# Performance work log

Hardware: AMD Instinct MI355X
Metric: run time of the kernel (lower is better)

Reference implementation:

```python
import jax, jax.numpy as jnp
import numpy as np

B = 2048        # graphs per batch
NC = 81         # cells per sudoku
IN_C, HID = 10, 128
N_ACT, N_NUM, N_TECH = 4, 9, 10


def _sudoku_edges():
    idx = np.arange(NC).reshape(9, 9)
    adj = np.zeros((NC, NC), dtype=bool)
    for i in range(9):
        for j in range(9):
            n = idx[i, j]
            adj[n, idx[i, :]] = True
            adj[n, idx[:, j]] = True
            bi, bj = 3 * (i // 3), 3 * (j // 3)
            adj[n, idx[bi:bi + 3, bj:bj + 3].reshape(-1)] = True
            adj[n, n] = False
    src, dst = np.nonzero(adj)  # 1620 directed edges
    return np.stack([src, dst]).astype(np.int32)


def setup_inputs() -> dict:
    key = jax.random.key(0)
    ks = jax.random.split(key, 12)
    N = B * NC
    base = _sudoku_edges()                          # [2, 1620]
    offs = (np.arange(B, dtype=np.int32) * NC)      # [B]
    ei = (base[:, None, :] + offs[None, :, None]).reshape(2, -1)  # [2, B*1620]
    batch = np.repeat(np.arange(B, dtype=np.int32), NC)           # [N]

    def lin(k, fan_in, fan_out):
        s = 1.0 / np.sqrt(fan_in)
        return jax.random.uniform(k, (fan_in, fan_out), jnp.float32, -s, s)

    return {
        "x": jax.random.normal(ks[0], (N, IN_C), jnp.float32),
        "edge_index": jnp.asarray(ei),
        "batch": jnp.asarray(batch),
        "W1": lin(ks[1], IN_C, HID), "b1": jnp.zeros((HID,), jnp.float32),
        "W2": lin(ks[2], HID, HID),  "b2": jnp.zeros((HID,), jnp.float32),
        "Wa": lin(ks[3], HID, N_ACT),  "ba": jnp.zeros((N_ACT,), jnp.float32),
        "Wc": lin(ks[4], HID, NC),     "bc": jnp.zeros((NC,), jnp.float32),
        "Wn": lin(ks[5], HID, N_NUM),  "bn": jnp.zeros((N_NUM,), jnp.float32),
        "Wt": lin(ks[6], HID, N_TECH), "bt": jnp.zeros((N_TECH,), jnp.float32),
    }


def _gcn_conv(x, edge_index, W, b):
    n = x.shape[0]
    loop = jnp.arange(n, dtype=edge_index.dtype)
    src = jnp.concatenate([edge_index[0], loop])
    dst = jnp.concatenate([edge_index[1], loop])
    deg = jax.ops.segment_sum(jnp.ones_like(dst, jnp.float32), dst, num_segments=n)
    dinv = jax.lax.rsqrt(deg)            # deg >= 1 due to self-loops
    norm = dinv[src] * dinv[dst]         # [E+N]
    h = x @ W                            # [N, out]
    msg = h[src] * norm[:, None]         # gather + scale
    return jax.ops.segment_sum(msg, dst, num_segments=n) + b


def reference(x, edge_index, batch, W1, b1, W2, b2, Wa, ba, Wc, bc, Wn, bn, Wt, bt):
    h = jax.nn.relu(_gcn_conv(x, edge_index, W1, b1))
    h = jax.nn.relu(_gcn_conv(h, edge_index, W2, b2))
    # global mean pool over graphs
    sums = jax.ops.segment_sum(h, batch, num_segments=B)
    cnts = jax.ops.segment_sum(jnp.ones((h.shape[0],), h.dtype), batch, num_segments=B)
    pooled = sums / jnp.maximum(cnts, 1.0)[:, None]   # [B, HID]
    return (pooled @ Wa + ba, pooled @ Wc + bc, pooled @ Wn + bn, pooled @ Wt + bt)
```

## Files before the change

kernel.cpp:

```cpp
#include <hip/hip_runtime.h>
#include <hip/hip_bf16.h>

typedef __attribute__((ext_vector_type(8))) short bf16x8;
typedef __attribute__((ext_vector_type(4))) float f32x4;

__device__ __forceinline__ unsigned short f2b(float f) {
    __hip_bfloat16 h = __float2bfloat16(f);
    return __builtin_bit_cast(unsigned short, h);
}
__device__ __forceinline__ float b2f(unsigned short u) {
    unsigned v = ((unsigned)u) << 16;
    return __builtin_bit_cast(float, v);
}
__device__ __forceinline__ float ldf(const void* p, int idx, bool f32) {
    return f32 ? ((const float*)p)[idx] : b2f(((const unsigned short*)p)[idx]);
}
__device__ __forceinline__ unsigned short ldb(const void* p, int idx, bool f32) {
    return f32 ? f2b(((const float*)p)[idx]) : ((const unsigned short*)p)[idx];
}
__device__ __forceinline__ int swz(int row, int col) {
    return row * 128 + (((col >> 3) ^ (row & 7)) << 3) + (col & 7);
}
__device__ __forceinline__ uint2 pk4(f32x4 c) {
    unsigned lo = (unsigned)f2b(c[0]) | ((unsigned)f2b(c[1]) << 16);
    unsigned hi = (unsigned)f2b(c[2]) | ((unsigned)f2b(c[3]) << 16);
    return make_uint2(lo, hi);
}
__device__ __forceinline__ bf16x8 mkB(uint2 a, uint2 b) {
    return __builtin_bit_cast(bf16x8, make_uint4(a.x, a.y, b.x, b.y));
}

__device__ __forceinline__ bool sniff_f32(const void* x) {
    const unsigned* p = (const unsigned*)x;
    int wild = 0;
#pragma unroll
    for (int i = 0; i < 16; ++i) {
        unsigned e = (p[i] >> 7) & 0xFF;
        wild += (e != 0 && (e < 0x68 || e > 0x90)) ? 1 : 0;
    }
    return wild > 8;
}

#define WS_B1F    16
#define WS_B2F    528
#define WS_BHF    1040
#define WS_W1R    1536
#define WS_W2R    9728
#define WS_SR     42496
#define WS_WH     60928

__global__ void k_repack(const void* __restrict__ x,
                         const void* __restrict__ W1, const void* __restrict__ b1,
                         const void* __restrict__ W2, const void* __restrict__ b2,
                         const void* __restrict__ Wa, const void* __restrict__ ba,
                         const void* __restrict__ Wc, const void* __restrict__ bc,
                         const void* __restrict__ Wn, const void* __restrict__ bn,
                         const void* __restrict__ Wt, const void* __restrict__ bt,
                         char* __restrict__ ws) {
    const bool f32 = sniff_f32(x);
    int idx = blockIdx.x * blockDim.x + threadIdx.x;
    if (idx < 4096) {
        int f = idx >> 5, k = idx & 31;
        unsigned short v = (k < 10) ? ldb(W1, k * 128 + f, f32) : (unsigned short)0;
        ((unsigned short*)(ws + WS_W1R))[idx] = v;
        return;
    }
    idx -= 4096;
    if (idx < 16384) {
        int f = idx >> 7, k = idx & 127;
        ((unsigned short*)(ws + WS_W2R))[idx] = ldb(W2, k * 128 + f, f32);
        return;
    }
    idx -= 16384;
    if (idx < 9216) {
        int fi = idx >> 9, rem = idx & 511;
        int lane = rem >> 3, j = rem & 7;
        int mt = fi / 3, s = fi - mt * 3;
        int node = mt * 16 + (lane & 15);
        int qa = lane >> 4;
        int cell = (2 * s + (j >> 2)) * 16 + qa * 4 + (j & 3);
        bool adj = false;
        if (node < 81 && cell < 81) {
            int ni = node / 9, nj = node % 9;
            int ci = cell / 9, cj = cell % 9;
            adj = (ni == ci) || (nj == cj) ||
                  ((ni / 3 == ci / 3) && (nj / 3 == cj / 3));
        }
        ((unsigned short*)(ws + WS_SR))[idx] = adj ? (unsigned short)0x3F80 : (unsigned short)0;
        return;
    }
    idx -= 9216;
    if (idx < 13312) {
        int i = idx / 416;
        int rem = idx - i * 416;
        int o = rem >> 2;
        int c = rem & 3;
        int f = i * 4 + c;
        const void* W; int oo, dim;
        if (o < 4)       { W = Wa; oo = o;      dim = 4;  }
        else if (o < 85) { W = Wc; oo = o - 4;  dim = 81; }
        else if (o < 94) { W = Wn; oo = o - 85; dim = 9;  }
        else             { W = Wt; oo = o - 94; dim = 10; }
        ((float*)(ws + WS_WH))[idx] = ldf(W, f * dim + oo, f32);
        return;
    }
    idx -= 13312;
    if (idx < 360) {
        float v;
        if (idx < 128)      v = ldf(b1, idx, f32);
        else if (idx < 256) v = ldf(b2, idx - 128, f32);
        else {
            int o = idx - 256;
            if (o < 4)       v = ldf(ba, o, f32);
            else if (o < 85) v = ldf(bc, o - 4, f32);
            else if (o < 94) v = ldf(bn, o - 85, f32);
            else             v = ldf(bt, o - 94, f32);
        }
        if (idx < 128)      ((float*)(ws + WS_B1F))[idx] = v;
        else if (idx < 256) ((float*)(ws + WS_B2F))[idx - 128] = v;
        else                ((float*)(ws + WS_BHF))[idx - 256] = v;
    }
}

__global__ __launch_bounds__(512, 4) void sudoku_gnn(
    const void* __restrict__ x, const char* __restrict__ ws,
    void* __restrict__ out, int nB)
{
    __shared__ __attribute__((aligned(16))) unsigned short hS[2][12288];
    __shared__ __attribute__((aligned(16))) unsigned short sS[9216];
    __shared__ float sPool[2][128];

    const bool f32 = sniff_f32(x);
    const unsigned short* w1r = (const unsigned short*)(ws + WS_W1R);
    const unsigned short* w2r = (const unsigned short*)(ws + WS_W2R);
    const float* b1f = (const float*)(ws + WS_B1F);
    const float* b2f = (const float*)(ws + WS_B2F);
    const float* bhf = (const float*)(ws + WS_BHF);
    const float* whf = (const float*)(ws + WS_WH);

    const int tid  = threadIdx.x;
    const int wave = tid >> 6;
    const int gq   = wave >> 2;
    const int lane = tid & 63;
    const int ln15 = lane & 15;
    const int q    = lane >> 4;
    const int k0   = q * 8;
    const int FB   = (wave & 3) * 32;
    const int g0   = blockIdx.x * 2;
    const bool hasB = (g0 + 1 < nB);
    const int g    = (g0 + gq < nB) ? g0 + gq : nB - 1;
    const float inv21 = 1.0f / 21.0f;
    const float inv81 = 1.0f / 81.0f;

    uint4 xr4[6]; unsigned xr1[6];
    if (!f32) {
        const char* xg = (const char*)x + (size_t)g * 1620;
#pragma unroll
        for (int mt = 0; mt < 6; ++mt) {
            int node = mt * 16 + ln15;
            uint4 r = {0, 0, 0, 0}; unsigned r1v = 0;
            if (node < 81) {
                if (q == 0)      r   = *(const uint4*)(xg + node * 20);
                else if (q == 1) r1v = *(const unsigned*)(xg + node * 20 + 16);
            }
            xr4[mt] = r; xr1[mt] = r1v;
        }
    }

    {
        const uint4* src = (const uint4*)(ws + WS_SR);
        uint4* dst = (uint4*)sS;
        for (int i = tid; i < 1152; i += 512) dst[i] = src[i];
    }

    bf16x8 w1f[2];
#pragma unroll
    for (int fmt = 0; fmt < 2; ++fmt)
        w1f[fmt] = *(const bf16x8*)&w1r[(FB + fmt * 16 + ln15) * 32 + k0];

    const f32x4 z4 = {0.f, 0.f, 0.f, 0.f};

    uint2 tpk[6][2];
#pragma unroll
    for (int mt = 0; mt < 6; ++mt) {
        bf16x8 xv = {0, 0, 0, 0, 0, 0, 0, 0};
        if (!f32) {
            if (q == 0)      xv = __builtin_bit_cast(bf16x8, xr4[mt]);
            else if (q == 1) { xv[0] = (short)(xr1[mt] & 0xFFFF); xv[1] = (short)(xr1[mt] >> 16); }
        } else {
            int node = mt * 16 + ln15;
            if (node < 81) {
                const float* xg = (const float*)x + (size_t)g * 810 + node * 10;
                if (q == 0) {
#pragma unroll
                    for (int j = 0; j < 8; ++j) xv[j] = (short)f2b(xg[j]);
                } else if (q == 1) {
                    xv[0] = (short)f2b(xg[8]);
                    xv[1] = (short)f2b(xg[9]);
                }
            }
        }
#pragma unroll
        for (int fmt = 0; fmt < 2; ++fmt)
            tpk[mt][fmt] = pk4(__builtin_amdgcn_mfma_f32_16x16x32_bf16(xv, w1f[fmt], z4, 0, 0, 0));
    }
    __syncthreads();

    f32x4 acc[6][2];

#pragma unroll
    for (int a = 0; a < 6; ++a)
#pragma unroll
        for (int c = 0; c < 2; ++c) acc[a][c] = z4;
    __builtin_amdgcn_s_setprio(1);
#pragma unroll
    for (int s = 0; s < 3; ++s) {
        bf16x8 B[2];
#pragma unroll
        for (int fmt = 0; fmt < 2; ++fmt)
            B[fmt] = mkB(tpk[2 * s][fmt], tpk[2 * s + 1][fmt]);
#pragma unroll
        for (int mt = 0; mt < 6; ++mt) {
            bf16x8 afr = *(const bf16x8*)&sS[((mt * 3 + s) * 64 + lane) * 8];
#pragma unroll
            for (int fmt = 0; fmt < 2; ++fmt)
                acc[mt][fmt] = __builtin_amdgcn_mfma_f32_16x16x32_bf16(afr, B[fmt], acc[mt][fmt], 0, 0, 0);
        }
    }
    __builtin_amdgcn_s_setprio(0);
#pragma unroll
    for (int fmt = 0; fmt < 2; ++fmt) {
        float bias = b1f[FB + fmt * 16 + ln15];
#pragma unroll
        for (int mt = 0; mt < 6; ++mt)
#pragma unroll
            for (int r = 0; r < 4; ++r) {
                int cell = mt * 16 + q * 4 + r;
                float v = fmaxf(acc[mt][fmt][r] * inv21 + bias, 0.0f);
                hS[gq][swz(cell, FB + fmt * 16 + ln15)] = f2b(v);
            }
    }
    __syncthreads();

#pragma unroll
    for (int a = 0; a < 6; ++a)
#pragma unroll
        for (int c = 0; c < 2; ++c) acc[a][c] = z4;
    __builtin_amdgcn_s_setprio(1);
#pragma unroll
    for (int kc = 0; kc < 4; ++kc) {
        bf16x8 w2f[2];
#pragma unroll
        for (int fmt = 0; fmt < 2; ++fmt)
            w2f[fmt] = *(const bf16x8*)&w2r[(FB + fmt * 16 + ln15) * 128 + kc * 32 + k0];
#pragma unroll
        for (int mt = 0; mt < 6; ++mt) {
            bf16x8 a3 = *(const bf16x8*)&hS[gq][swz(mt * 16 + ln15, kc * 32 + k0)];
#pragma unroll
            for (int fmt = 0; fmt < 2; ++fmt)
                acc[mt][fmt] = __builtin_amdgcn_mfma_f32_16x16x32_bf16(a3, w2f[fmt], acc[mt][fmt], 0, 0, 0);
        }
    }
    __builtin_amdgcn_s_setprio(0);
#pragma unroll
    for (int mt = 0; mt < 6; ++mt)
#pragma unroll
        for (int fmt = 0; fmt < 2; ++fmt)
            tpk[mt][fmt] = pk4(acc[mt][fmt]);

#pragma unroll
    for (int a = 0; a < 6; ++a)
#pragma unroll
        for (int c = 0; c < 2; ++c) acc[a][c] = z4;
    __builtin_amdgcn_s_setprio(1);
#pragma unroll
    for (int s = 0; s < 3; ++s) {
        bf16x8 B[2];
#pragma unroll
        for (int fmt = 0; fmt < 2; ++fmt)
            B[fmt] = mkB(tpk[2 * s][fmt], tpk[2 * s + 1][fmt]);
#pragma unroll
        for (int mt = 0; mt < 6; ++mt) {
            bf16x8 afr = *(const bf16x8*)&sS[((mt * 3 + s) * 64 + lane) * 8];
#pragma unroll
            for (int fmt = 0; fmt < 2; ++fmt)
                acc[mt][fmt] = __builtin_amdgcn_mfma_f32_16x16x32_bf16(afr, B[fmt], acc[mt][fmt], 0, 0, 0);
        }
    }
    __builtin_amdgcn_s_setprio(0);
#pragma unroll
    for (int fmt = 0; fmt < 2; ++fmt) {
        float bias = b2f[FB + fmt * 16 + ln15];
        float sum = 0.f;
#pragma unroll
        for (int mt = 0; mt < 6; ++mt)
#pragma unroll
            for (int r = 0; r < 4; ++r) {
                int cell = mt * 16 + q * 4 + r;
                float v = fmaxf(acc[mt][fmt][r] * inv21 + bias, 0.0f);
                sum += (cell < 81) ? v : 0.0f;
            }
        sum += __shfl_xor(sum, 16);
        sum += __shfl_xor(sum, 32);
        if (lane < 16) sPool[gq][FB + fmt * 16 + lane] = sum * inv81;
    }
    __syncthreads();

    if (tid < 416) {
        int pr = tid >> 1, hf = tid & 1;
        int gg = (pr >= 104) ? 1 : 0;
        int o  = pr - gg * 104;
        int gh = g0 + gg;
        float a = 0.0f;
        if (gg == 0 || hasB) {
            a = hf ? 0.0f : bhf[o];
            const float4* wh4 = (const float4*)whf;
            const float4* sp4 = (const float4*)sPool[gg];
#pragma unroll
            for (int ii = 0; ii < 16; ++ii) {
                int i = hf * 16 + ii;
                float4 wv = wh4[i * 104 + o];
                float4 pv = sp4[i];
                a += pv.x * wv.x + pv.y * wv.y + pv.z * wv.z + pv.w * wv.w;
            }
        }
        a += __shfl_xor(a, 1);
        if (hf == 0 && (gg == 0 || hasB)) {
            int oo; size_t off;
            if (o < 4)       { oo = o;      off = (size_t)gh * 4 + oo; }
            else if (o < 85) { oo = o - 4;  off = (size_t)nB * 4  + (size_t)gh * 81 + oo; }
            else if (o < 94) { oo = o - 85; off = (size_t)nB * 85 + (size_t)gh * 9  + oo; }
            else             { oo = o - 94; off = (size_t)nB * 94 + (size_t)gh * 10 + oo; }
            if (f32) ((float*)out)[off] = a;
            else     ((unsigned short*)out)[off] = f2b(a);
        }
    }
}

extern "C" void kernel_launch(void* const* d_in, const int* in_sizes, int n_in,
                              void* d_out, int out_size, void* d_ws, size_t ws_size,
                              hipStream_t stream) {
    const void* x  = d_in[0];
    int nB = in_sizes[2] / 81;
    if (nB <= 0) return;

    char* ws = (char*)d_ws;
    hipLaunchKernelGGL(k_repack, dim3(170), dim3(256), 0, stream,
                       x, d_in[3], d_in[4], d_in[5], d_in[6],
                       d_in[7], d_in[8], d_in[9], d_in[10],
                       d_in[11], d_in[12], d_in[13], d_in[14], ws);
    hipLaunchKernelGGL(sudoku_gnn, dim3((nB + 1) / 2), dim3(512), 0, stream,
                       x, (const char*)ws, d_out, nB);
}
```

Baseline: 132.8 us.

## Drop repack kernel; read weights directly and build adjacency in-kernel

Removes the separate weight-repacking launch and has the main GNN kernel read W1, W2, biases and head weights straight from the inputs, converting on the fly. The sudoku adjacency tile is now computed per block in shared memory instead of copied from a workspace. This saves a kernel launch and the dependency between the two kernels. In exchange, every block does scalar strided gathers of W2 and the head weights, which are uncoalesced, plus extra integer arithmetic.

```diff
diff --git a/kernel.cpp b/kernel.cpp
--- a/kernel.cpp
+++ b/kernel.cpp
@@ -41,89 +41,14 @@
     return wild > 8;
 }
 
-#define WS_B1F    16
-#define WS_B2F    528
-#define WS_BHF    1040
-#define WS_W1R    1536
-#define WS_W2R    9728
-#define WS_SR     42496
-#define WS_WH     60928
-
-__global__ void k_repack(const void* __restrict__ x,
-                         const void* __restrict__ W1, const void* __restrict__ b1,
-                         const void* __restrict__ W2, const void* __restrict__ b2,
-                         const void* __restrict__ Wa, const void* __restrict__ ba,
-                         const void* __restrict__ Wc, const void* __restrict__ bc,
-                         const void* __restrict__ Wn, const void* __restrict__ bn,
-                         const void* __restrict__ Wt, const void* __restrict__ bt,
-                         char* __restrict__ ws) {
-    const bool f32 = sniff_f32(x);
-    int idx = blockIdx.x * blockDim.x + threadIdx.x;
-    if (idx < 4096) {
-        int f = idx >> 5, k = idx & 31;
-        unsigned short v = (k < 10) ? ldb(W1, k * 128 + f, f32) : (unsigned short)0;
-        ((unsigned short*)(ws + WS_W1R))[idx] = v;
-        return;
-    }
-    idx -= 4096;
-    if (idx < 16384) {
-        int f = idx >> 7, k = idx & 127;
-        ((unsigned short*)(ws + WS_W2R))[idx] = ldb(W2, k * 128 + f, f32);
-        return;
-    }
-    idx -= 16384;
-    if (idx < 9216) {
-        int fi = idx >> 9, rem = idx & 511;
-        int lane = rem >> 3, j = rem & 7;
-        int mt = fi / 3, s = fi - mt * 3;
-        int node = mt * 16 + (lane & 15);
-        int qa = lane >> 4;
-        int cell = (2 * s + (j >> 2)) * 16 + qa * 4 + (j & 3);
-        bool adj = false;
-        if (node < 81 && cell < 81) {
-            int ni = node / 9, nj = node % 9;
-            int ci = cell / 9, cj = cell % 9;
-            adj = (ni == ci) || (nj == cj) ||
-                  ((ni / 3 == ci / 3) && (nj / 3 == cj / 3));
-        }
-        ((unsigned short*)(ws + WS_SR))[idx] = adj ? (unsigned short)0x3F80 : (unsigned short)0;
-        return;
-    }
-    idx -= 9216;
-    if (idx < 13312) {
-        int i = idx / 416;
-        int rem = idx - i * 416;
-        int o = rem >> 2;
-        int c = rem & 3;
-        int f = i * 4 + c;
-        const void* W; int oo, dim;
-        if (o < 4)       { W = Wa; oo = o;      dim = 4;  }
-        else if (o < 85) { W = Wc; oo = o - 4;  dim = 81; }
-        else if (o < 94) { W = Wn; oo = o - 85; dim = 9;  }
-        else             { W = Wt; oo = o - 94; dim = 10; }
-        ((float*)(ws + WS_WH))[idx] = ldf(W, f * dim + oo, f32);
-        return;
-    }
-    idx -= 13312;
-    if (idx < 360) {
-        float v;
-        if (idx < 128)      v = ldf(b1, idx, f32);
-        else if (idx < 256) v = ldf(b2, idx - 128, f32);
-        else {
-            int o = idx - 256;
-            if (o < 4)       v = ldf(ba, o, f32);
-            else if (o < 85) v = ldf(bc, o - 4, f32);
-            else if (o < 94) v = ldf(bn, o - 85, f32);
-            else             v = ldf(bt, o - 94, f32);
-        }
-        if (idx < 128)      ((float*)(ws + WS_B1F))[idx] = v;
-        else if (idx < 256) ((float*)(ws + WS_B2F))[idx - 128] = v;
-        else                ((float*)(ws + WS_BHF))[idx - 256] = v;
-    }
-}
-
 __global__ __launch_bounds__(512, 4) void sudoku_gnn(
-    const void* __restrict__ x, const char* __restrict__ ws,
+    const void* __restrict__ x,
+    const void* __restrict__ W1, const void* __restrict__ b1,
+    const void* __restrict__ W2, const void* __restrict__ b2,
+    const void* __restrict__ Wa, const void* __restrict__ ba,
+    const void* __restrict__ Wc, const void* __restrict__ bc,
+    const void* __restrict__ Wn, const void* __restrict__ bn,
+    const void* __restrict__ Wt, const void* __restrict__ bt,
     void* __restrict__ out, int nB)
 {
     __shared__ __attribute__((aligned(16))) unsigned short hS[2][12288];
@@ -131,12 +56,6 @@
     __shared__ float sPool[2][128];
 
     const bool f32 = sniff_f32(x);
-    const unsigned short* w1r = (const unsigned short*)(ws + WS_W1R);
-    const unsigned short* w2r = (const unsigned short*)(ws + WS_W2R);
-    const float* b1f = (const float*)(ws + WS_B1F);
-    const float* b2f = (const float*)(ws + WS_B2F);
-    const float* bhf = (const float*)(ws + WS_BHF);
-    const float* whf = (const float*)(ws + WS_WH);
 
     const int tid  = threadIdx.x;
     const int wave = tid >> 6;
@@ -168,15 +87,38 @@
     }
 
     {
-        const uint4* src = (const uint4*)(ws + WS_SR);
-        uint4* dst = (uint4*)sS;
-        for (int i = tid; i < 1152; i += 512) dst[i] = src[i];
+#pragma unroll
+        for (int it = 0; it < 18; ++it) {
+            int idx = tid + it * 512;
+            int fi = idx >> 9, rem = idx & 511;
+            int ln_ = rem >> 3, j = rem & 7;
+            int mt = fi / 3, s = fi - mt * 3;
+            int node = mt * 16 + (ln_ & 15);
+            int qa = ln_ >> 4;
+            int cell = (2 * s + (j >> 2)) * 16 + qa * 4 + (j & 3);
+            bool adj = false;
+            if (node < 81 && cell < 81) {
+                int ni = node / 9, nj = node - ni * 9;
+                int ci = cell / 9, cj = cell - ci * 9;
+                adj = (ni == ci) || (nj == cj) ||
+                      ((ni / 3 == ci / 3) && (nj / 3 == cj / 3));
+            }
+            sS[idx] = adj ? (unsigned short)0x3F80 : (unsigned short)0;
+        }
     }
 
     bf16x8 w1f[2];
 #pragma unroll
-    for (int fmt = 0; fmt < 2; ++fmt)
-        w1f[fmt] = *(const bf16x8*)&w1r[(FB + fmt * 16 + ln15) * 32 + k0];
+    for (int fmt = 0; fmt < 2; ++fmt) {
+        bf16x8 v = {0, 0, 0, 0, 0, 0, 0, 0};
+        int f = FB + fmt * 16 + ln15;
+#pragma unroll
+        for (int j = 0; j < 8; ++j) {
+            int k = k0 + j;
+            if (k < 10) v[j] = (short)ldb(W1, k * 128 + f, f32);
+        }
+        w1f[fmt] = v;
+    }
 
     const f32x4 z4 = {0.f, 0.f, 0.f, 0.f};
 
@@ -230,7 +172,7 @@
     __builtin_amdgcn_s_setprio(0);
 #pragma unroll
     for (int fmt = 0; fmt < 2; ++fmt) {
-        float bias = b1f[FB + fmt * 16 + ln15];
+        float bias = ldf(b1, FB + fmt * 16 + ln15, f32);
 #pragma unroll
         for (int mt = 0; mt < 6; ++mt)
 #pragma unroll
@@ -251,8 +193,14 @@
     for (int kc = 0; kc < 4; ++kc) {
         bf16x8 w2f[2];
 #pragma unroll
-        for (int fmt = 0; fmt < 2; ++fmt)
-            w2f[fmt] = *(const bf16x8*)&w2r[(FB + fmt * 16 + ln15) * 128 + kc * 32 + k0];
+        for (int fmt = 0; fmt < 2; ++fmt) {
+            bf16x8 v;
+            int f = FB + fmt * 16 + ln15;
+#pragma unroll
+            for (int j = 0; j < 8; ++j)
+                v[j] = (short)ldb(W2, (kc * 32 + k0 + j) * 128 + f, f32);
+            w2f[fmt] = v;
+        }
 #pragma unroll
         for (int mt = 0; mt < 6; ++mt) {
             bf16x8 a3 = *(const bf16x8*)&hS[gq][swz(mt * 16 + ln15, kc * 32 + k0)];
@@ -290,7 +238,7 @@
     __builtin_amdgcn_s_setprio(0);
 #pragma unroll
     for (int fmt = 0; fmt < 2; ++fmt) {
-        float bias = b2f[FB + fmt * 16 + ln15];
+        float bias = ldf(b2, FB + fmt * 16 + ln15, f32);
         float sum = 0.f;
 #pragma unroll
         for (int mt = 0; mt < 6; ++mt)
@@ -313,24 +261,31 @@
         int gh = g0 + gg;
         float a = 0.0f;
         if (gg == 0 || hasB) {
-            a = hf ? 0.0f : bhf[o];
-            const float4* wh4 = (const float4*)whf;
+            const void* W; const void* bb; int oo, dim;
+            if (o < 4)       { W = Wa; bb = ba; oo = o;      dim = 4;  }
+            else if (o < 85) { W = Wc; bb = bc; oo = o - 4;  dim = 81; }
+            else if (o < 94) { W = Wn; bb = bn; oo = o - 85; dim = 9;  }
+            else             { W = Wt; bb = bt; oo = o - 94; dim = 10; }
+            a = hf ? 0.0f : ldf(bb, oo, f32);
             const float4* sp4 = (const float4*)sPool[gg];
 #pragma unroll
             for (int ii = 0; ii < 16; ++ii) {
                 int i = hf * 16 + ii;
-                float4 wv = wh4[i * 104 + o];
                 float4 pv = sp4[i];
-                a += pv.x * wv.x + pv.y * wv.y + pv.z * wv.z + pv.w * wv.w;
+                float w0 = ldf(W, (4 * i + 0) * dim + oo, f32);
+                float w1v = ldf(W, (4 * i + 1) * dim + oo, f32);
+                float w2v = ldf(W, (4 * i + 2) * dim + oo, f32);
+                float w3 = ldf(W, (4 * i + 3) * dim + oo, f32);
+                a += pv.x * w0 + pv.y * w1v + pv.z * w2v + pv.w * w3;
             }
         }
         a += __shfl_xor(a, 1);
         if (hf == 0 && (gg == 0 || hasB)) {
-            int oo; size_t off;
-            if (o < 4)       { oo = o;      off = (size_t)gh * 4 + oo; }
-            else if (o < 85) { oo = o - 4;  off = (size_t)nB * 4  + (size_t)gh * 81 + oo; }
-            else if (o < 94) { oo = o - 85; off = (size_t)nB * 85 + (size_t)gh * 9  + oo; }
-            else             { oo = o - 94; off = (size_t)nB * 94 + (size_t)gh * 10 + oo; }
+            int oo2; size_t off;
+            if (o < 4)       { oo2 = o;      off = (size_t)gh * 4 + oo2; }
+            else if (o < 85) { oo2 = o - 4;  off = (size_t)nB * 4  + (size_t)gh * 81 + oo2; }
+            else if (o < 94) { oo2 = o - 85; off = (size_t)nB * 85 + (size_t)gh * 9  + oo2; }
+            else             { oo2 = o - 94; off = (size_t)nB * 94 + (size_t)gh * 10 + oo2; }
             if (f32) ((float*)out)[off] = a;
             else     ((unsigned short*)out)[off] = f2b(a);
         }
@@ -344,11 +299,9 @@
     int nB = in_sizes[2] / 81;
     if (nB <= 0) return;
 
-    char* ws = (char*)d_ws;
-    hipLaunchKernelGGL(k_repack, dim3(170), dim3(256), 0, stream,
+    hipLaunchKernelGGL(sudoku_gnn, dim3((nB + 1) / 2), dim3(512), 0, stream,
                        x, d_in[3], d_in[4], d_in[5], d_in[6],
                        d_in[7], d_in[8], d_in[9], d_in[10],
-                       d_in[11], d_in[12], d_in[13], d_in[14], ws);
-    hipLaunchKernelGGL(sudoku_gnn, dim3((nB + 1) / 2), dim3(512), 0, stream,
-                       x, (const char*)ws, d_out, nB);
-}
+                       d_in[11], d_in[12], d_in[13], d_in[14],
+                       d_out, nB);
+}
```

After: 171.8 us. 29.3% more time.

## Process four graphs per block with prefetch of second pair's inputs

Applied to the files above, without the earlier changes.

Each block now handles two pairs of graphs in sequence instead of one pair, halving the grid. The second pair's node features are loaded into registers while the first pair is still being computed, and the shared adjacency matrix is staged into LDS once per block instead of once per pair. The cost is more registers per thread, which may lower occupancy, and fewer blocks, which gives less parallelism across CUs. A missing __syncthreads between the first pair's pooled-head read of sPool/hS and the second pair's writes could be a race.

```diff
diff --git a/kernel.cpp b/kernel.cpp
--- a/kernel.cpp
+++ b/kernel.cpp
@@ -146,15 +146,17 @@
     const int q    = lane >> 4;
     const int k0   = q * 8;
     const int FB   = (wave & 3) * 32;
-    const int g0   = blockIdx.x * 2;
-    const bool hasB = (g0 + 1 < nB);
-    const int g    = (g0 + gq < nB) ? g0 + gq : nB - 1;
+    const int g0   = blockIdx.x * 4;
+    const int gA   = (g0 + gq < nB) ? g0 + gq : nB - 1;
+    const int gB   = (g0 + 2 + gq < nB) ? g0 + 2 + gq : nB - 1;
     const float inv21 = 1.0f / 21.0f;
     const float inv81 = 1.0f / 81.0f;
 
+    const f32x4 z4 = {0.f, 0.f, 0.f, 0.f};
+
     uint4 xr4[6]; unsigned xr1[6];
     if (!f32) {
-        const char* xg = (const char*)x + (size_t)g * 1620;
+        const char* xg = (const char*)x + (size_t)gA * 1620;
 #pragma unroll
         for (int mt = 0; mt < 6; ++mt) {
             int node = mt * 16 + ln15;
@@ -177,8 +179,6 @@
 #pragma unroll
     for (int fmt = 0; fmt < 2; ++fmt)
         w1f[fmt] = *(const bf16x8*)&w1r[(FB + fmt * 16 + ln15) * 32 + k0];
-
-    const f32x4 z4 = {0.f, 0.f, 0.f, 0.f};
 
     uint2 tpk[6][2];
 #pragma unroll
@@ -190,7 +190,7 @@
         } else {
             int node = mt * 16 + ln15;
             if (node < 81) {
-                const float* xg = (const float*)x + (size_t)g * 810 + node * 10;
+                const float* xg = (const float*)x + (size_t)gA * 810 + node * 10;
                 if (q == 0) {
 #pragma unroll
                     for (int j = 0; j < 8; ++j) xv[j] = (short)f2b(xg[j]);
@@ -203,6 +203,21 @@
 #pragma unroll
         for (int fmt = 0; fmt < 2; ++fmt)
             tpk[mt][fmt] = pk4(__builtin_amdgcn_mfma_f32_16x16x32_bf16(xv, w1f[fmt], z4, 0, 0, 0));
+    }
+
+    uint4 pr4[6]; unsigned pr1[6];
+    if (!f32) {
+        const char* xg = (const char*)x + (size_t)gB * 1620;
+#pragma unroll
+        for (int mt = 0; mt < 6; ++mt) {
+            int node = mt * 16 + ln15;
+            uint4 r = {0, 0, 0, 0}; unsigned r1v = 0;
+            if (node < 81) {
+                if (q == 0)      r   = *(const uint4*)(xg + node * 20);
+                else if (q == 1) r1v = *(const unsigned*)(xg + node * 20 + 16);
+            }
+            pr4[mt] = r; pr1[mt] = r1v;
+        }
     }
     __syncthreads();
 
@@ -312,7 +327,7 @@
         int o  = pr - gg * 104;
         int gh = g0 + gg;
         float a = 0.0f;
-        if (gg == 0 || hasB) {
+        if (gh < nB) {
             a = hf ? 0.0f : bhf[o];
             const float4* wh4 = (const float4*)whf;
             const float4* sp4 = (const float4*)sPool[gg];
@@ -325,7 +340,7 @@
             }
         }
         a += __shfl_xor(a, 1);
-        if (hf == 0 && (gg == 0 || hasB)) {
+        if (hf == 0 && gh < nB) {
             int oo; size_t off;
             if (o < 4)       { oo = o;      off = (size_t)gh * 4 + oo; }
             else if (o < 85) { oo = o - 4;  off = (size_t)nB * 4  + (size_t)gh * 81 + oo; }
@@ -335,6 +350,158 @@
             else     ((unsigned short*)out)[off] = f2b(a);
         }
     }
+
+#pragma unroll
+    for (int mt = 0; mt < 6; ++mt) {
+        bf16x8 xv = {0, 0, 0, 0, 0, 0, 0, 0};
+        if (!f32) {
+            if (q == 0)      xv = __builtin_bit_cast(bf16x8, pr4[mt]);
+            else if (q == 1) { xv[0] = (short)(pr1[mt] & 0xFFFF); xv[1] = (short)(pr1[mt] >> 16); }
+        } else {
+            int node = mt * 16 + ln15;
+            if (node < 81) {
+                const float* xg = (const float*)x + (size_t)gB * 810 + node * 10;
+                if (q == 0) {
+#pragma unroll
+                    for (int j = 0; j < 8; ++j) xv[j] = (short)f2b(xg[j]);
+                } else if (q == 1) {
+                    xv[0] = (short)f2b(xg[8]);
+                    xv[1] = (short)f2b(xg[9]);
+                }
+            }
+        }
+#pragma unroll
+        for (int fmt = 0; fmt < 2; ++fmt)
+            tpk[mt][fmt] = pk4(__builtin_amdgcn_mfma_f32_16x16x32_bf16(xv, w1f[fmt], z4, 0, 0, 0));
+    }
+
+#pragma unroll
+    for (int a = 0; a < 6; ++a)
+#pragma unroll
+        for (int c = 0; c < 2; ++c) acc[a][c] = z4;
+    __builtin_amdgcn_s_setprio(1);
+#pragma unroll
+    for (int s = 0; s < 3; ++s) {
+        bf16x8 B[2];
+#pragma unroll
+        for (int fmt = 0; fmt < 2; ++fmt)
+            B[fmt] = mkB(tpk[2 * s][fmt], tpk[2 * s + 1][fmt]);
+#pragma unroll
+        for (int mt = 0; mt < 6; ++mt) {
+            bf16x8 afr = *(const bf16x8*)&sS[((mt * 3 + s) * 64 + lane) * 8];
+#pragma unroll
+            for (int fmt = 0; fmt < 2; ++fmt)
+                acc[mt][fmt] = __builtin_amdgcn_mfma_f32_16x16x32_bf16(afr, B[fmt], acc[mt][fmt], 0, 0, 0);
+        }
+    }
+    __builtin_amdgcn_s_setprio(0);
+#pragma unroll
+    for (int fmt = 0; fmt < 2; ++fmt) {
+        float bias = b1f[FB + fmt * 16 + ln15];
+#pragma unroll
+        for (int mt = 0; mt < 6; ++mt)
+#pragma unroll
+            for (int r = 0; r < 4; ++r) {
+                int cell = mt * 16 + q * 4 + r;
+                float v = fmaxf(acc[mt][fmt][r] * inv21 + bias, 0.0f);
+                hS[gq][swz(cell, FB + fmt * 16 + ln15)] = f2b(v);
+            }
+    }
+    __syncthreads();
+
+#pragma unroll
+    for (int a = 0; a < 6; ++a)
+#pragma unroll
+        for (int c = 0; c < 2; ++c) acc[a][c] = z4;
+    __builtin_amdgcn_s_setprio(1);
+#pragma unroll
+    for (int kc = 0; kc < 4; ++kc) {
+        bf16x8 w2f[2];
+#pragma unroll
+        for (int fmt = 0; fmt < 2; ++fmt)
+            w2f[fmt] = *(const bf16x8*)&w2r[(FB + fmt * 16 + ln15) * 128 + kc * 32 + k0];
+#pragma unroll
+        for (int mt = 0; mt < 6; ++mt) {
+            bf16x8 a3 = *(const bf16x8*)&hS[gq][swz(mt * 16 + ln15, kc * 32 + k0)];
+#pragma unroll
+            for (int fmt = 0; fmt < 2; ++fmt)
+                acc[mt][fmt] = __builtin_amdgcn_mfma_f32_16x16x32_bf16(a3, w2f[fmt], acc[mt][fmt], 0, 0, 0);
+        }
+    }
+    __builtin_amdgcn_s_setprio(0);
+#pragma unroll
+    for (int mt = 0; mt < 6; ++mt)
+#pragma unroll
+        for (int fmt = 0; fmt < 2; ++fmt)
+            tpk[mt][fmt] = pk4(acc[mt][fmt]);
+
+#pragma unroll
+    for (int a = 0; a < 6; ++a)
+#pragma unroll
+        for (int c = 0; c < 2; ++c) acc[a][c] = z4;
+    __builtin_amdgcn_s_setprio(1);
+#pragma unroll
+    for (int s = 0; s < 3; ++s) {
+        bf16x8 B[2];
+#pragma unroll
+        for (int fmt = 0; fmt < 2; ++fmt)
+            B[fmt] = mkB(tpk[2 * s][fmt], tpk[2 * s + 1][fmt]);
+#pragma unroll
+        for (int mt = 0; mt < 6; ++mt) {
+            bf16x8 afr = *(const bf16x8*)&sS[((mt * 3 + s) * 64 + lane) * 8];
+#pragma unroll
+            for (int fmt = 0; fmt < 2; ++fmt)
+                acc[mt][fmt] = __builtin_amdgcn_mfma_f32_16x16x32_bf16(afr, B[fmt], acc[mt][fmt], 0, 0, 0);
+        }
+    }
+    __builtin_amdgcn_s_setprio(0);
+#pragma unroll
+    for (int fmt = 0; fmt < 2; ++fmt) {
+        float bias = b2f[FB + fmt * 16 + ln15];
+        float sum = 0.f;
+#pragma unroll
+        for (int mt = 0; mt < 6; ++mt)
+#pragma unroll
+            for (int r = 0; r < 4; ++r) {
+                int cell = mt * 16 + q * 4 + r;
+                float v = fmaxf(acc[mt][fmt][r] * inv21 + bias, 0.0f);
+                sum += (cell < 81) ? v : 0.0f;
+            }
+        sum += __shfl_xor(sum, 16);
+        sum += __shfl_xor(sum, 32);
+        if (lane < 16) sPool[gq][FB + fmt * 16 + lane] = sum * inv81;
+    }
+    __syncthreads();
+
+    if (tid < 416) {
+        int pr = tid >> 1, hf = tid & 1;
+        int gg = (pr >= 104) ? 1 : 0;
+        int o  = pr - gg * 104;
+        int gh = g0 + 2 + gg;
+        float a = 0.0f;
+        if (gh < nB) {
+            a = hf ? 0.0f : bhf[o];
+            const float4* wh4 = (const float4*)whf;
+            const float4* sp4 = (const float4*)sPool[gg];
+#pragma unroll
+            for (int ii = 0; ii < 16; ++ii) {
+                int i = hf * 16 + ii;
+                float4 wv = wh4[i * 104 + o];
+                float4 pv = sp4[i];
+                a += pv.x * wv.x + pv.y * wv.y + pv.z * wv.z + pv.w * wv.w;
+            }
+        }
+        a += __shfl_xor(a, 1);
+        if (hf == 0 && gh < nB) {
+            int oo; size_t off;
+            if (o < 4)       { oo = o;      off = (size_t)gh * 4 + oo; }
+            else if (o < 85) { oo = o - 4;  off = (size_t)nB * 4  + (size_t)gh * 81 + oo; }
+            else if (o < 94) { oo = o - 85; off = (size_t)nB * 85 + (size_t)gh * 9  + oo; }
+            else             { oo = o - 94; off = (size_t)nB * 94 + (size_t)gh * 10 + oo; }
+            if (f32) ((float*)out)[off] = a;
+            else     ((unsigned short*)out)[off] = f2b(a);
+        }
+    }
 }
 
 extern "C" void kernel_launch(void* const* d_in, const int* in_sizes, int n_in,
@@ -349,6 +516,6 @@
                        x, d_in[3], d_in[4], d_in[5], d_in[6],
                        d_in[7], d_in[8], d_in[9], d_in[10],
                        d_in[11], d_in[12], d_in[13], d_in[14], ws);
-    hipLaunchKernelGGL(sudoku_gnn, dim3((nB + 1) / 2), dim3(512), 0, stream,
+    hipLaunchKernelGGL(sudoku_gnn, dim3((nB + 3) / 4), dim3(512), 0, stream,
                        x, (const char*)ws, d_out, nB);
 }
```

Measured after the change: 150.0 us. +12.9%, slower.
